# Performance work log

Hardware: AMD Instinct MI355X
Metric: run time of the kernel (lower is better)

Reference implementation:

```python
import jax, jax.numpy as jnp
import numpy as np

DIM = 256
HEADS = 4
DIM_HEAD = 32
HIDDEN = HEADS * DIM_HEAD  # 128
SCALE = DIM_HEAD ** -0.5
EPS = 1e-5


def setup_inputs() -> dict:
    key = jax.random.key(0)
    ks = jax.random.split(key, 6)
    b, h, w = 4, 64, 64
    x = jax.random.normal(ks[0], (b, DIM, h, w), dtype=jnp.float32)
    # GroupNorm(1, dim) affine params
    gamma = jnp.ones((DIM,), dtype=jnp.float32)
    beta = jnp.zeros((DIM,), dtype=jnp.float32)
    # 1x1 convs as dense matrices over channels
    w_qkv = jax.random.normal(ks[1], (3 * HIDDEN, DIM), dtype=jnp.float32) * (DIM ** -0.5)
    w_out = jax.random.normal(ks[2], (DIM, HIDDEN), dtype=jnp.float32) * (HIDDEN ** -0.5)
    b_out = jax.random.normal(ks[3], (DIM,), dtype=jnp.float32) * 0.02
    return {"x": x, "gamma": gamma, "beta": beta, "w_qkv": w_qkv,
            "w_out": w_out, "b_out": b_out}


def reference(x, gamma, beta, w_qkv, w_out, b_out):
    b, c, h, w = x.shape
    n = h * w
    # GroupNorm with 1 group == layernorm over (C,H,W) per sample, per-channel affine
    mu = jnp.mean(x, axis=(1, 2, 3), keepdims=True)
    var = jnp.var(x, axis=(1, 2, 3), keepdims=True)
    xn = (x - mu) * jax.lax.rsqrt(var + EPS)
    xn = xn * gamma[None, :, None, None] + beta[None, :, None, None]
    # 1x1 conv -> qkv, then split into heads; flatten spatial dims to n = h*w
    qkv = jnp.einsum('bchw,oc->bohw', xn, w_qkv)            # (b, 3*hidden, h, w)
    qkv = qkv.reshape(b, 3, HEADS, DIM_HEAD, n)
    q, k, v = qkv[:, 0], qkv[:, 1], qkv[:, 2]               # (b, heads, dim_head, n)
    q = q * SCALE
    sim = jnp.einsum('bhci,bhcj->bhij', q, k)               # (b, heads, n, n)
    attn = jax.nn.softmax(sim, axis=-1)                     # stable softmax (max subtract)
    out = jnp.einsum('bhij,bhcj->bhic', attn, v)            # (b, heads, n, dim_head)
    out = out.transpose(0, 1, 3, 2).reshape(b, HIDDEN, h, w)
    y = jnp.einsum('bchw,oc->bohw', out, w_out) + b_out[None, :, None, None]
    return y
```

## Files before the change

kernel.cpp:

```cpp
#include <hip/hip_runtime.h>
#include <math.h>

#define BATCH 4
#define CDIM 256
#define NPIX 4096
#define NPB (CDIM * NPIX)
#define HEADS 4
#define DH 32
#define HID 128
#define OQKV 384
#define QK_SCALE (0.1767766952966369f * 1.44269504088896340736f)
#define SOFTMAX_C 10.0f
#define LN_EPS 1e-5f

typedef _Float16 f16;
typedef _Float16 f16x8 __attribute__((ext_vector_type(8)));
typedef _Float16 f16x4 __attribute__((ext_vector_type(4)));
typedef float f32x4 __attribute__((ext_vector_type(4)));

__device__ __forceinline__ void gload16(const void* g, void* l) {
  __builtin_amdgcn_global_load_lds(
      (const __attribute__((address_space(1))) void*)g,
      (__attribute__((address_space(3))) void*)l, 16, 0, 0);
}

union U8u { unsigned int u[4]; f16x8 v; };
union U8h { f16 h[8]; f16x8 v; };

__global__ __launch_bounds__(256) void ln_reduce(const float* __restrict__ x,
                                                 float* __restrict__ part) {
  const int blk = blockIdx.x;
  const int b = blk >> 6;
  const int slice = blk & 63;
  const float4* xp = (const float4*)(x + (size_t)b * NPB) + (size_t)slice * 4096;
  const int t = threadIdx.x;
  float s = 0.f, ss = 0.f;
#pragma unroll
  for (int k = 0; k < 16; ++k) {
    float4 v = xp[t + k * 256];
    s += v.x + v.y + v.z + v.w;
    ss += v.x * v.x + v.y * v.y + v.z * v.z + v.w * v.w;
  }
#pragma unroll
  for (int d = 1; d < 64; d <<= 1) {
    s += __shfl_xor(s, d);
    ss += __shfl_xor(ss, d);
  }
  __shared__ float red[8];
  const int wv = t >> 6;
  if ((t & 63) == 0) { red[wv * 2] = s; red[wv * 2 + 1] = ss; }
  __syncthreads();
  if (t == 0) {
    part[blk * 2]     = red[0] + red[2] + red[4] + red[6];
    part[blk * 2 + 1] = red[1] + red[3] + red[5] + red[7];
  }
}

__global__ void ln_finalize(const float* __restrict__ part, float* __restrict__ stats) {
  const int t = threadIdx.x;
  const int b = t >> 6, lane = t & 63;
  float s  = part[(b * 64 + lane) * 2];
  float ss = part[(b * 64 + lane) * 2 + 1];
#pragma unroll
  for (int d = 1; d < 64; d <<= 1) {
    s += __shfl_xor(s, d);
    ss += __shfl_xor(ss, d);
  }
  if (lane == 0) {
    float mu = s * (1.f / (float)NPB);
    float var = ss * (1.f / (float)NPB) - mu * mu;
    stats[b * 2] = mu;
    stats[b * 2 + 1] = rsqrtf(var + LN_EPS);
  }
}

__global__ __launch_bounds__(256) void qkv_gemm(const float* __restrict__ x,
                                                const float* __restrict__ gamma,
                                                const float* __restrict__ beta,
                                                const float* __restrict__ wqkv,
                                                const float* __restrict__ stats,
                                                f16* __restrict__ qT,
                                                f16* __restrict__ kT,
                                                f16* __restrict__ vO) {
  const int b = blockIdx.z;
  const int oclass = blockIdx.y;
  const int p0 = blockIdx.x * 128;
  const int t = threadIdx.x;
  const int w = t >> 6, lane = t & 63, low4 = lane & 15, quad = lane >> 4;
  const int ow0 = (w >> 1) * 64, pw0 = (w & 1) * 64;
  const float mu = stats[2 * b], rstd = stats[2 * b + 1];
  const float wscale = (oclass == 0) ? QK_SCALE : 1.f;

  __shared__ f16 Ws[128 * 40];
  __shared__ float Xs[32 * 132];

  const int wo = t >> 1, wh = (t & 1) * 16;
  const int xc = t >> 3, xpq = (t & 7) * 16;
  const float* wg = wqkv + (size_t)(oclass * 128 + wo) * CDIM + wh;
  const float* xg = x + ((size_t)b * CDIM + xc) * NPIX + p0 + xpq;

  f32x4 acc[4][4] = {};
  f32x4 wr[4], xr[4];
  {
    const float ga = gamma[xc] * rstd;
    const float bb = beta[xc] - mu * ga;
#pragma unroll
    for (int j = 0; j < 4; ++j) {
      wr[j] = *(const f32x4*)(wg + j * 4);
      f32x4 r = *(const f32x4*)(xg + j * 4);
      r[0] = r[0] * ga + bb; r[1] = r[1] * ga + bb;
      r[2] = r[2] * ga + bb; r[3] = r[3] * ga + bb;
      xr[j] = r;
    }
  }

  for (int ks = 0; ks < 8; ++ks) {
    __syncthreads();
    {
      U8h h0, h1;
#pragma unroll
      for (int e = 0; e < 4; ++e) {
        h0.h[e]     = (f16)(wr[0][e] * wscale);
        h0.h[4 + e] = (f16)(wr[1][e] * wscale);
        h1.h[e]     = (f16)(wr[2][e] * wscale);
        h1.h[4 + e] = (f16)(wr[3][e] * wscale);
      }
      *(f16x8*)&Ws[wo * 40 + wh]     = h0.v;
      *(f16x8*)&Ws[wo * 40 + wh + 8] = h1.v;
#pragma unroll
      for (int j = 0; j < 4; ++j)
        *(f32x4*)&Xs[xc * 132 + xpq + 4 * j] = xr[j];
    }
    __syncthreads();

    if (ks < 7) {
      const int k0n = (ks + 1) * 32;
      const float ga = gamma[k0n + xc] * rstd;
      const float bb = beta[k0n + xc] - mu * ga;
#pragma unroll
      for (int j = 0; j < 4; ++j) {
        wr[j] = *(const f32x4*)(wg + k0n + j * 4);
        f32x4 r = *(const f32x4*)(xg + (size_t)k0n * NPIX + j * 4);
        r[0] = r[0] * ga + bb; r[1] = r[1] * ga + bb;
        r[2] = r[2] * ga + bb; r[3] = r[3] * ga + bb;
        xr[j] = r;
      }
    }

    f16x8 wf[4], xf[4];
#pragma unroll
    for (int i = 0; i < 4; ++i)
      wf[i] = *(const f16x8*)&Ws[(ow0 + i * 16 + low4) * 40 + quad * 8];
#pragma unroll
    for (int j = 0; j < 4; ++j) {
      const int pl = pw0 + j * 16 + low4;
      U8u xv;
#pragma unroll
      for (int r = 0; r < 4; ++r) {
        const float e0 = Xs[(quad * 8 + 2 * r) * 132 + pl];
        const float e1 = Xs[(quad * 8 + 2 * r + 1) * 132 + pl];
        xv.u[r] = __builtin_bit_cast(unsigned int,
                    __builtin_amdgcn_cvt_pkrtz(e0, e1));
      }
      xf[j] = xv.v;
    }

    if (oclass < 2) {
#pragma unroll
      for (int i = 0; i < 4; ++i)
#pragma unroll
        for (int j = 0; j < 4; ++j)
          acc[i][j] = __builtin_amdgcn_mfma_f32_16x16x32_f16(wf[i], xf[j], acc[i][j], 0, 0, 0);
    } else {
#pragma unroll
      for (int i = 0; i < 4; ++i)
#pragma unroll
        for (int j = 0; j < 4; ++j)
          acc[i][j] = __builtin_amdgcn_mfma_f32_16x16x32_f16(xf[i], wf[j], acc[i][j], 0, 0, 0);
    }
  }

  if (oclass < 2) {
    f16* dst = (oclass == 0) ? qT : kT;
#pragma unroll
    for (int i = 0; i < 4; ++i) {
      const int o_loc = ow0 + i * 16 + quad * 4;
      const int hh = o_loc >> 5;
      const int cb = o_loc & 31;
      f16* base = dst + ((size_t)(b * HEADS + hh) * NPIX) * DH + cb;
#pragma unroll
      for (int j = 0; j < 4; ++j) {
        const int p = p0 + pw0 + j * 16 + low4;
        f16x4 v = {(f16)acc[i][j][0], (f16)acc[i][j][1],
                   (f16)acc[i][j][2], (f16)acc[i][j][3]};
        *(f16x4*)(base + (size_t)p * DH) = v;
      }
    }
  } else {
#pragma unroll
    for (int j = 0; j < 4; ++j) {
      const int o_loc = ow0 + j * 16 + low4;
      const int hh = o_loc >> 5;
      const int cc = o_loc & 31;
      f16* base = vO + ((size_t)(b * HEADS + hh) * DH + cc) * NPIX;
#pragma unroll
      for (int i = 0; i < 4; ++i) {
        const int p = p0 + pw0 + i * 16 + quad * 4;
        f16x4 v = {(f16)acc[i][j][0], (f16)acc[i][j][1],
                   (f16)acc[i][j][2], (f16)acc[i][j][3]};
        *(f16x4*)(base + p) = v;
      }
    }
  }
}

__global__ __launch_bounds__(256, 4) void attn_kernel(const f16* __restrict__ qT,
                                                      const f16* __restrict__ kT,
                                                      const f16* __restrict__ vO,
                                                      f16* __restrict__ obufT) {
  const int bh_idx = blockIdx.x;
  const int i0 = blockIdx.y * 64;
  const int h = bh_idx & 3;
  const int b = bh_idx >> 2;
  const int t = threadIdx.x;
  const int w = t >> 6;
  const int lane = t & 63;
  const int low4 = lane & 15;
  const int quad = lane >> 4;

  __shared__ f16 Ks[2][2048];
  __shared__ f16 Vs[2][2048];

  const size_t bh = (size_t)(b * HEADS + h);
  const f16* kTb = kT + bh * NPIX * DH;
  const f16* vb  = vO + bh * DH * NPIX;

  const int vn = w * 64 + lane;
  const int vc = vn >> 3;
  const int vjc = (vn & 7) ^ (vc & 7);
  const f16* vgbase = vb + (size_t)vc * NPIX + vjc * 8;
  const int krow = w * 16 + (lane >> 2);
  const int kchk = (lane & 3) ^ ((lane >> 3) & 3);
  const f16* kgbase = kTb + (size_t)krow * DH + kchk * 8;

  const f16x8 qf = *(const f16x8*)(qT + (bh * NPIX + i0 + w * 16 + low4) * DH + quad * 8);

  f32x4 ov0 = {0, 0, 0, 0}, ov1 = {0, 0, 0, 0};
  float lp = 0.f;
  const f32x4 cinit = {-SOFTMAX_C, -SOFTMAX_C, -SOFTMAX_C, -SOFTMAX_C};

  union U4 { unsigned int u[2]; f16x4 v; };

  auto stage = [&](int buf, int jt) {
    gload16(kgbase + (size_t)jt * DH, &Ks[buf][w * 512]);
    gload16(vgbase + jt,              &Vs[buf][w * 512]);
  };

  const int kread_chunk = (quad ^ ((low4 >> 1) & 3)) << 3;

  stage(0, 0);
  for (int it = 0; it < NPIX / 64; ++it) {
    const int cur = it & 1;
    __syncthreads();
    if (it + 1 < NPIX / 64) stage(cur ^ 1, (it + 1) * 64);

    f16x8 kf[4];
#pragma unroll
    for (int tt = 0; tt < 4; ++tt)
      kf[tt] = *(const f16x8*)&Ks[cur][(tt * 16 + low4) * 32 + kread_chunk];
    f16x4 va[4][2];
#pragma unroll
    for (int tt = 0; tt < 4; ++tt) {
      const int jc16 = tt * 2 + (quad >> 1);
      const int sub = (quad & 1) * 4;
      const int c0 = low4, c1 = low4 + 16;
      va[tt][0] = *(const f16x4*)&Vs[cur][(c0 * 8 + (jc16 ^ (c0 & 7))) * 8 + sub];
      va[tt][1] = *(const f16x4*)&Vs[cur][(c1 * 8 + (jc16 ^ (c1 & 7))) * 8 + sub];
    }

    f32x4 st[4];
    __builtin_amdgcn_s_setprio(1);
#pragma unroll
    for (int tt = 0; tt < 4; ++tt)
      st[tt] = __builtin_amdgcn_mfma_f32_16x16x32_f16(kf[tt], qf, cinit, 0, 0, 0);
    __builtin_amdgcn_s_setprio(0);

    U4 pb[4];
#pragma unroll
    for (int tt = 0; tt < 4; ++tt) {
      const float a0 = __builtin_amdgcn_exp2f(st[tt][0]);
      const float a1 = __builtin_amdgcn_exp2f(st[tt][1]);
      const float a2 = __builtin_amdgcn_exp2f(st[tt][2]);
      const float a3 = __builtin_amdgcn_exp2f(st[tt][3]);
      lp += (a0 + a1) + (a2 + a3);
      pb[tt].u[0] = __builtin_bit_cast(unsigned int, __builtin_amdgcn_cvt_pkrtz(a0, a1));
      pb[tt].u[1] = __builtin_bit_cast(unsigned int, __builtin_amdgcn_cvt_pkrtz(a2, a3));
    }

    __builtin_amdgcn_s_setprio(1);
#pragma unroll
    for (int tt = 0; tt < 4; ++tt) {
      ov0 = __builtin_amdgcn_mfma_f32_16x16x16f16(va[tt][0], pb[tt].v, ov0, 0, 0, 0);
      ov1 = __builtin_amdgcn_mfma_f32_16x16x16f16(va[tt][1], pb[tt].v, ov1, 0, 0, 0);
    }
    __builtin_amdgcn_s_setprio(0);
  }

  lp += __shfl_xor(lp, 16);
  lp += __shfl_xor(lp, 32);
  const float inv = 1.f / lp;

  const int pix0 = i0 + w * 16 + low4;
  f16* ob = obufT + ((size_t)b * NPIX + pix0) * HID + h * DH + 4 * quad;
  {
    f16x4 v0 = {(f16)(ov0[0] * inv), (f16)(ov0[1] * inv), (f16)(ov0[2] * inv), (f16)(ov0[3] * inv)};
    f16x4 v1 = {(f16)(ov1[0] * inv), (f16)(ov1[1] * inv), (f16)(ov1[2] * inv), (f16)(ov1[3] * inv)};
    *(f16x4*)(ob)      = v0;
    *(f16x4*)(ob + 16) = v1;
  }
}

__global__ __launch_bounds__(256) void out_gemm(const f16* __restrict__ obufT,
                                                const float* __restrict__ wout,
                                                const float* __restrict__ bout,
                                                float* __restrict__ y) {
  const int b = blockIdx.z;
  const int o0 = blockIdx.y * 128;
  const int p0 = blockIdx.x * 128;
  const int t = threadIdx.x;
  const int w = t >> 6, lane = t & 63, low4 = lane & 15, quad = lane >> 4;
  const int ow0 = (w >> 1) * 64, pw0 = (w & 1) * 64;

  __shared__ f16 Ws2[128 * 136];

  {
    const int ro = t >> 1, half = (t & 1) * 64;
    const float* wg = wout + (size_t)(o0 + ro) * HID + half;
#pragma unroll
    for (int jj = 0; jj < 8; ++jj) {
      f32x4 a = *(const f32x4*)(wg + jj * 8);
      f32x4 c = *(const f32x4*)(wg + jj * 8 + 4);
      U8h hv;
      hv.h[0]=(f16)a[0]; hv.h[1]=(f16)a[1]; hv.h[2]=(f16)a[2]; hv.h[3]=(f16)a[3];
      hv.h[4]=(f16)c[0]; hv.h[5]=(f16)c[1]; hv.h[6]=(f16)c[2]; hv.h[7]=(f16)c[3];
      *(f16x8*)&Ws2[ro * 136 + half + jj * 8] = hv.v;
    }
  }
  __syncthreads();

  const f16* bg = obufT + ((size_t)b * NPIX + p0) * HID;

  f32x4 acc[4][4] = {};
#pragma unroll
  for (int ks = 0; ks < 4; ++ks) {
    const int k0 = ks * 32;
    f16x8 af[4], bf[4];
#pragma unroll
    for (int j = 0; j < 4; ++j)
      bf[j] = *(const f16x8*)(bg + (size_t)(pw0 + j * 16 + low4) * HID + k0 + quad * 8);
#pragma unroll
    for (int i = 0; i < 4; ++i)
      af[i] = *(const f16x8*)&Ws2[(ow0 + i * 16 + low4) * 136 + k0 + quad * 8];
#pragma unroll
    for (int i = 0; i < 4; ++i)
#pragma unroll
      for (int j = 0; j < 4; ++j)
        acc[i][j] = __builtin_amdgcn_mfma_f32_16x16x32_f16(af[i], bf[j], acc[i][j], 0, 0, 0);
  }

#pragma unroll
  for (int i = 0; i < 4; ++i) {
    const int ob = o0 + ow0 + i * 16 + quad * 4;
    const float b0v = bout[ob], b1v = bout[ob + 1], b2v = bout[ob + 2], b3v = bout[ob + 3];
    float* yb = y + ((size_t)b * CDIM + ob) * NPIX + p0 + pw0 + low4;
#pragma unroll
    for (int j = 0; j < 4; ++j) {
      yb[j * 16]                       = acc[i][j][0] + b0v;
      yb[(size_t)NPIX + j * 16]       = acc[i][j][1] + b1v;
      yb[(size_t)2 * NPIX + j * 16]   = acc[i][j][2] + b2v;
      yb[(size_t)3 * NPIX + j * 16]   = acc[i][j][3] + b3v;
    }
  }
}

extern "C" void kernel_launch(void* const* d_in, const int* in_sizes, int n_in,
                              void* d_out, int out_size, void* d_ws, size_t ws_size,
                              hipStream_t stream) {
  const float* x     = (const float*)d_in[0];
  const float* gamma = (const float*)d_in[1];
  const float* beta  = (const float*)d_in[2];
  const float* wqkv  = (const float*)d_in[3];
  const float* wout  = (const float*)d_in[4];
  const float* bout  = (const float*)d_in[5];
  float* y = (float*)d_out;

  char* wsb = (char*)d_ws;
  float* part  = (float*)wsb;
  float* stats = part + 512;
  f16* qT = (f16*)(wsb + 4096);
  f16* kT = qT + (size_t)BATCH * HEADS * NPIX * DH;
  f16* vO = kT + (size_t)BATCH * HEADS * NPIX * DH;
  f16* obufT = vO + (size_t)BATCH * HEADS * NPIX * DH;

  ln_reduce<<<dim3(256), 256, 0, stream>>>(x, part);
  ln_finalize<<<dim3(1), 256, 0, stream>>>(part, stats);
  qkv_gemm<<<dim3(32, 3, BATCH), 256, 0, stream>>>(x, gamma, beta, wqkv, stats, qT, kT, vO);
  attn_kernel<<<dim3(16, 64), 256, 0, stream>>>(qT, kT, vO, obufT);
  out_gemm<<<dim3(32, 2, BATCH), 256, 0, stream>>>(obufT, wout, bout, y);
}
```

Measured before the change: 159.8 us.

## Split attention keys across waves with register-direct loads and LDS combine

Each wave now takes a quarter of the key/value sequence for all 64 queries of the block, instead of every wave sweeping all keys for its own 16 queries. K and V fragments are loaded straight from global memory into double-buffered registers, which removes the LDS staging and the per-tile __syncthreads. Partial outputs and row sums from the four waves are reduced through shared memory at the end. The trade-offs are more registers (launch bounds lowered to 3) and less coalesced global loads that depend on the L2 cache rather than on LDS reuse.

```diff
diff --git a/kernel.cpp b/kernel.cpp
--- a/kernel.cpp
+++ b/kernel.cpp
@@ -214,7 +214,7 @@
   }
 }
 
-__global__ __launch_bounds__(256, 4) void attn_kernel(const f16* __restrict__ qT,
+__global__ __launch_bounds__(256, 3) void attn_kernel(const f16* __restrict__ qT,
                                                       const f16* __restrict__ kT,
                                                       const f16* __restrict__ vO,
                                                       f16* __restrict__ obufT) {
@@ -228,93 +228,107 @@
   const int low4 = lane & 15;
   const int quad = lane >> 4;
 
-  __shared__ f16 Ks[2][2048];
-  __shared__ f16 Vs[2][2048];
-
   const size_t bh = (size_t)(b * HEADS + h);
   const f16* kTb = kT + bh * NPIX * DH;
   const f16* vb  = vO + bh * DH * NPIX;
 
-  const int vn = w * 64 + lane;
-  const int vc = vn >> 3;
-  const int vjc = (vn & 7) ^ (vc & 7);
-  const f16* vgbase = vb + (size_t)vc * NPIX + vjc * 8;
-  const int krow = w * 16 + (lane >> 2);
-  const int kchk = (lane & 3) ^ ((lane >> 3) & 3);
-  const f16* kgbase = kTb + (size_t)krow * DH + kchk * 8;
-
-  const f16x8 qf = *(const f16x8*)(qT + (bh * NPIX + i0 + w * 16 + low4) * DH + quad * 8);
-
-  f32x4 ov0 = {0, 0, 0, 0}, ov1 = {0, 0, 0, 0};
-  float lp = 0.f;
+  f16x8 qf[4];
+#pragma unroll
+  for (int qg = 0; qg < 4; ++qg)
+    qf[qg] = *(const f16x8*)(qT + (bh * NPIX + i0 + qg * 16 + low4) * DH + quad * 8);
+
+  f32x4 ov[4][2] = {};
+  float lp[4] = {0.f, 0.f, 0.f, 0.f};
   const f32x4 cinit = {-SOFTMAX_C, -SOFTMAX_C, -SOFTMAX_C, -SOFTMAX_C};
 
   union U4 { unsigned int u[2]; f16x4 v; };
 
-  auto stage = [&](int buf, int jt) {
-    gload16(kgbase + (size_t)jt * DH, &Ks[buf][w * 512]);
-    gload16(vgbase + jt,              &Vs[buf][w * 512]);
-  };
-
-  const int kread_chunk = (quad ^ ((low4 >> 1) & 3)) << 3;
-
-  stage(0, 0);
-  for (int it = 0; it < NPIX / 64; ++it) {
-    const int cur = it & 1;
-    __syncthreads();
-    if (it + 1 < NPIX / 64) stage(cur ^ 1, (it + 1) * 64);
-
-    f16x8 kf[4];
-#pragma unroll
-    for (int tt = 0; tt < 4; ++tt)
-      kf[tt] = *(const f16x8*)&Ks[cur][(tt * 16 + low4) * 32 + kread_chunk];
-    f16x4 va[4][2];
-#pragma unroll
-    for (int tt = 0; tt < 4; ++tt) {
-      const int jc16 = tt * 2 + (quad >> 1);
-      const int sub = (quad & 1) * 4;
-      const int c0 = low4, c1 = low4 + 16;
-      va[tt][0] = *(const f16x4*)&Vs[cur][(c0 * 8 + (jc16 ^ (c0 & 7))) * 8 + sub];
-      va[tt][1] = *(const f16x4*)&Vs[cur][(c1 * 8 + (jc16 ^ (c1 & 7))) * 8 + sub];
-    }
-
-    f32x4 st[4];
-    __builtin_amdgcn_s_setprio(1);
-#pragma unroll
-    for (int tt = 0; tt < 4; ++tt)
-      st[tt] = __builtin_amdgcn_mfma_f32_16x16x32_f16(kf[tt], qf, cinit, 0, 0, 0);
-    __builtin_amdgcn_s_setprio(0);
-
-    U4 pb[4];
-#pragma unroll
-    for (int tt = 0; tt < 4; ++tt) {
-      const float a0 = __builtin_amdgcn_exp2f(st[tt][0]);
-      const float a1 = __builtin_amdgcn_exp2f(st[tt][1]);
-      const float a2 = __builtin_amdgcn_exp2f(st[tt][2]);
-      const float a3 = __builtin_amdgcn_exp2f(st[tt][3]);
-      lp += (a0 + a1) + (a2 + a3);
-      pb[tt].u[0] = __builtin_bit_cast(unsigned int, __builtin_amdgcn_cvt_pkrtz(a0, a1));
-      pb[tt].u[1] = __builtin_bit_cast(unsigned int, __builtin_amdgcn_cvt_pkrtz(a2, a3));
-    }
-
-    __builtin_amdgcn_s_setprio(1);
-#pragma unroll
-    for (int tt = 0; tt < 4; ++tt) {
-      ov0 = __builtin_amdgcn_mfma_f32_16x16x16f16(va[tt][0], pb[tt].v, ov0, 0, 0, 0);
-      ov1 = __builtin_amdgcn_mfma_f32_16x16x16f16(va[tt][1], pb[tt].v, ov1, 0, 0, 0);
-    }
-    __builtin_amdgcn_s_setprio(0);
-  }
-
-  lp += __shfl_xor(lp, 16);
-  lp += __shfl_xor(lp, 32);
-  const float inv = 1.f / lp;
-
-  const int pix0 = i0 + w * 16 + low4;
-  f16* ob = obufT + ((size_t)b * NPIX + pix0) * HID + h * DH + 4 * quad;
+  const int j0w = w * (NPIX / 4);
+  const f16* kg  = kTb + (size_t)(j0w + low4) * DH + quad * 8;
+  const f16* vg0 = vb + (size_t)low4 * NPIX + j0w + quad * 4;
+  const f16* vg1 = vb + (size_t)(16 + low4) * NPIX + j0w + quad * 4;
+
+  f16x8 kf[2][2];
+  f16x4 va[2][2][2];
+  kf[0][0] = *(const f16x8*)(kg);
+  kf[0][1] = *(const f16x8*)(kg + (size_t)16 * DH);
+  va[0][0][0] = *(const f16x4*)(vg0);
+  va[0][1][0] = *(const f16x4*)(vg0 + 16);
+  va[0][0][1] = *(const f16x4*)(vg1);
+  va[0][1][1] = *(const f16x4*)(vg1 + 16);
+
+#pragma unroll 2
+  for (int it = 0; it < 32; ++it) {
+    const int cb = it & 1;
+    if (it + 1 < 32) {
+      const int off = (it + 1) * 32;
+      kf[cb ^ 1][0] = *(const f16x8*)(kg + (size_t)off * DH);
+      kf[cb ^ 1][1] = *(const f16x8*)(kg + (size_t)(off + 16) * DH);
+      va[cb ^ 1][0][0] = *(const f16x4*)(vg0 + off);
+      va[cb ^ 1][1][0] = *(const f16x4*)(vg0 + off + 16);
+      va[cb ^ 1][0][1] = *(const f16x4*)(vg1 + off);
+      va[cb ^ 1][1][1] = *(const f16x4*)(vg1 + off + 16);
+    }
+
+#pragma unroll
+    for (int qg = 0; qg < 4; ++qg) {
+      f32x4 st0 = __builtin_amdgcn_mfma_f32_16x16x32_f16(kf[cb][0], qf[qg], cinit, 0, 0, 0);
+      f32x4 st1 = __builtin_amdgcn_mfma_f32_16x16x32_f16(kf[cb][1], qf[qg], cinit, 0, 0, 0);
+
+      U4 pb0, pb1;
+      const float a0 = __builtin_amdgcn_exp2f(st0[0]);
+      const float a1 = __builtin_amdgcn_exp2f(st0[1]);
+      const float a2 = __builtin_amdgcn_exp2f(st0[2]);
+      const float a3 = __builtin_amdgcn_exp2f(st0[3]);
+      lp[qg] += (a0 + a1) + (a2 + a3);
+      pb0.u[0] = __builtin_bit_cast(unsigned int, __builtin_amdgcn_cvt_pkrtz(a0, a1));
+      pb0.u[1] = __builtin_bit_cast(unsigned int, __builtin_amdgcn_cvt_pkrtz(a2, a3));
+      const float b0 = __builtin_amdgcn_exp2f(st1[0]);
+      const float b1 = __builtin_amdgcn_exp2f(st1[1]);
+      const float b2 = __builtin_amdgcn_exp2f(st1[2]);
+      const float b3 = __builtin_amdgcn_exp2f(st1[3]);
+      lp[qg] += (b0 + b1) + (b2 + b3);
+      pb1.u[0] = __builtin_bit_cast(unsigned int, __builtin_amdgcn_cvt_pkrtz(b0, b1));
+      pb1.u[1] = __builtin_bit_cast(unsigned int, __builtin_amdgcn_cvt_pkrtz(b2, b3));
+
+      ov[qg][0] = __builtin_amdgcn_mfma_f32_16x16x16f16(va[cb][0][0], pb0.v, ov[qg][0], 0, 0, 0);
+      ov[qg][0] = __builtin_amdgcn_mfma_f32_16x16x16f16(va[cb][1][0], pb1.v, ov[qg][0], 0, 0, 0);
+      ov[qg][1] = __builtin_amdgcn_mfma_f32_16x16x16f16(va[cb][0][1], pb0.v, ov[qg][1], 0, 0, 0);
+      ov[qg][1] = __builtin_amdgcn_mfma_f32_16x16x16f16(va[cb][1][1], pb1.v, ov[qg][1], 0, 0, 0);
+    }
+  }
+
+#pragma unroll
+  for (int qg = 0; qg < 4; ++qg) {
+    lp[qg] += __shfl_xor(lp[qg], 16);
+    lp[qg] += __shfl_xor(lp[qg], 32);
+  }
+
+  __shared__ float Cmb[4][2048];
+  __shared__ float Lps[4][4][16];
+#pragma unroll
+  for (int qg = 0; qg < 4; ++qg) {
+#pragma unroll
+    for (int ch = 0; ch < 2; ++ch)
+      *(f32x4*)&Cmb[w][((qg * 2 + ch) * 64 + lane) * 4] = ov[qg][ch];
+    if (quad == 0) Lps[w][qg][low4] = lp[qg];
+  }
+  __syncthreads();
+
+  const float lpt = ((Lps[0][w][low4] + Lps[1][w][low4]) +
+                     (Lps[2][w][low4] + Lps[3][w][low4]));
+  const float inv = 1.f / lpt;
+  f32x4 o0 = {0, 0, 0, 0}, o1 = {0, 0, 0, 0};
+#pragma unroll
+  for (int u = 0; u < 4; ++u) {
+    o0 += *(const f32x4*)&Cmb[u][((w * 2 + 0) * 64 + lane) * 4];
+    o1 += *(const f32x4*)&Cmb[u][((w * 2 + 1) * 64 + lane) * 4];
+  }
+
+  f16* ob = obufT + ((size_t)b * NPIX + i0 + w * 16 + low4) * HID + h * DH + 4 * quad;
   {
-    f16x4 v0 = {(f16)(ov0[0] * inv), (f16)(ov0[1] * inv), (f16)(ov0[2] * inv), (f16)(ov0[3] * inv)};
-    f16x4 v1 = {(f16)(ov1[0] * inv), (f16)(ov1[1] * inv), (f16)(ov1[2] * inv), (f16)(ov1[3] * inv)};
+    f16x4 v0 = {(f16)(o0[0] * inv), (f16)(o0[1] * inv), (f16)(o0[2] * inv), (f16)(o0[3] * inv)};
+    f16x4 v1 = {(f16)(o1[0] * inv), (f16)(o1[1] * inv), (f16)(o1[2] * inv), (f16)(o1[3] * inv)};
     *(f16x4*)(ob)      = v0;
     *(f16x4*)(ob + 16) = v1;
   }
```

New measurement: 196.6 us. +23.0%, slower.

## Split key tiles across waves and reduce partial attention outputs in LDS

Applied to the files above, without the earlier changes.

Each wave now owns a 16-key slice of every 64-key tile for all 64 queries, instead of owning 16 queries over all keys. This cuts per-wave LDS reads of K and V by a factor of four. The cost is holding four Q fragments and eight output accumulators per wave, plus a cross-wave reduction of partial outputs and row sums through LDS at the end. Register pressure rises, which may hurt occupancy under the 4-blocks launch bound.

```diff
diff --git a/kernel.cpp b/kernel.cpp
--- a/kernel.cpp
+++ b/kernel.cpp
@@ -228,8 +228,11 @@
   const int low4 = lane & 15;
   const int quad = lane >> 4;
 
-  __shared__ f16 Ks[2][2048];
-  __shared__ f16 Vs[2][2048];
+  union SharedU {
+    struct { f16 Ks[2][2048]; f16 Vs[2][2048]; } s;
+    struct { float Cmb[4][8][256]; float Lps[4][4][16]; } c;
+  };
+  __shared__ SharedU sh;
 
   const size_t bh = (size_t)(b * HEADS + h);
   const f16* kTb = kT + bh * NPIX * DH;
@@ -243,20 +246,27 @@
   const int kchk = (lane & 3) ^ ((lane >> 3) & 3);
   const f16* kgbase = kTb + (size_t)krow * DH + kchk * 8;
 
-  const f16x8 qf = *(const f16x8*)(qT + (bh * NPIX + i0 + w * 16 + low4) * DH + quad * 8);
-
-  f32x4 ov0 = {0, 0, 0, 0}, ov1 = {0, 0, 0, 0};
-  float lp = 0.f;
+  f16x8 qf[4];
+#pragma unroll
+  for (int qg = 0; qg < 4; ++qg)
+    qf[qg] = *(const f16x8*)(qT + (bh * NPIX + i0 + qg * 16 + low4) * DH + quad * 8);
+
+  f32x4 ov[4][2] = {};
+  float lp[4] = {0.f, 0.f, 0.f, 0.f};
   const f32x4 cinit = {-SOFTMAX_C, -SOFTMAX_C, -SOFTMAX_C, -SOFTMAX_C};
 
   union U4 { unsigned int u[2]; f16x4 v; };
 
   auto stage = [&](int buf, int jt) {
-    gload16(kgbase + (size_t)jt * DH, &Ks[buf][w * 512]);
-    gload16(vgbase + jt,              &Vs[buf][w * 512]);
+    gload16(kgbase + (size_t)jt * DH, &sh.s.Ks[buf][w * 512]);
+    gload16(vgbase + jt,              &sh.s.Vs[buf][w * 512]);
   };
 
-  const int kread_chunk = (quad ^ ((low4 >> 1) & 3)) << 3;
+  const int kread_off = (w * 16 + low4) * 32 + ((quad ^ ((low4 >> 1) & 3)) << 3);
+  const int jc16 = w * 2 + (quad >> 1);
+  const int sub = (quad & 1) * 4;
+  const int va_off0 = (low4 * 8 + (jc16 ^ (low4 & 7))) * 8 + sub;
+  const int va_off1 = ((16 + low4) * 8 + (jc16 ^ ((16 + low4) & 7))) * 8 + sub;
 
   stage(0, 0);
   for (int it = 0; it < NPIX / 64; ++it) {
@@ -264,57 +274,68 @@
     __syncthreads();
     if (it + 1 < NPIX / 64) stage(cur ^ 1, (it + 1) * 64);
 
-    f16x8 kf[4];
-#pragma unroll
-    for (int tt = 0; tt < 4; ++tt)
-      kf[tt] = *(const f16x8*)&Ks[cur][(tt * 16 + low4) * 32 + kread_chunk];
-    f16x4 va[4][2];
-#pragma unroll
-    for (int tt = 0; tt < 4; ++tt) {
-      const int jc16 = tt * 2 + (quad >> 1);
-      const int sub = (quad & 1) * 4;
-      const int c0 = low4, c1 = low4 + 16;
-      va[tt][0] = *(const f16x4*)&Vs[cur][(c0 * 8 + (jc16 ^ (c0 & 7))) * 8 + sub];
-      va[tt][1] = *(const f16x4*)&Vs[cur][(c1 * 8 + (jc16 ^ (c1 & 7))) * 8 + sub];
-    }
+    const f16x8 kf  = *(const f16x8*)&sh.s.Ks[cur][kread_off];
+    const f16x4 va0 = *(const f16x4*)&sh.s.Vs[cur][va_off0];
+    const f16x4 va1 = *(const f16x4*)&sh.s.Vs[cur][va_off1];
 
     f32x4 st[4];
     __builtin_amdgcn_s_setprio(1);
 #pragma unroll
-    for (int tt = 0; tt < 4; ++tt)
-      st[tt] = __builtin_amdgcn_mfma_f32_16x16x32_f16(kf[tt], qf, cinit, 0, 0, 0);
+    for (int qg = 0; qg < 4; ++qg)
+      st[qg] = __builtin_amdgcn_mfma_f32_16x16x32_f16(kf, qf[qg], cinit, 0, 0, 0);
     __builtin_amdgcn_s_setprio(0);
 
     U4 pb[4];
 #pragma unroll
-    for (int tt = 0; tt < 4; ++tt) {
-      const float a0 = __builtin_amdgcn_exp2f(st[tt][0]);
-      const float a1 = __builtin_amdgcn_exp2f(st[tt][1]);
-      const float a2 = __builtin_amdgcn_exp2f(st[tt][2]);
-      const float a3 = __builtin_amdgcn_exp2f(st[tt][3]);
-      lp += (a0 + a1) + (a2 + a3);
-      pb[tt].u[0] = __builtin_bit_cast(unsigned int, __builtin_amdgcn_cvt_pkrtz(a0, a1));
-      pb[tt].u[1] = __builtin_bit_cast(unsigned int, __builtin_amdgcn_cvt_pkrtz(a2, a3));
+    for (int qg = 0; qg < 4; ++qg) {
+      const float a0 = __builtin_amdgcn_exp2f(st[qg][0]);
+      const float a1 = __builtin_amdgcn_exp2f(st[qg][1]);
+      const float a2 = __builtin_amdgcn_exp2f(st[qg][2]);
+      const float a3 = __builtin_amdgcn_exp2f(st[qg][3]);
+      lp[qg] += (a0 + a1) + (a2 + a3);
+      pb[qg].u[0] = __builtin_bit_cast(unsigned int, __builtin_amdgcn_cvt_pkrtz(a0, a1));
+      pb[qg].u[1] = __builtin_bit_cast(unsigned int, __builtin_amdgcn_cvt_pkrtz(a2, a3));
     }
 
     __builtin_amdgcn_s_setprio(1);
 #pragma unroll
-    for (int tt = 0; tt < 4; ++tt) {
-      ov0 = __builtin_amdgcn_mfma_f32_16x16x16f16(va[tt][0], pb[tt].v, ov0, 0, 0, 0);
-      ov1 = __builtin_amdgcn_mfma_f32_16x16x16f16(va[tt][1], pb[tt].v, ov1, 0, 0, 0);
+    for (int qg = 0; qg < 4; ++qg) {
+      ov[qg][0] = __builtin_amdgcn_mfma_f32_16x16x16f16(va0, pb[qg].v, ov[qg][0], 0, 0, 0);
+      ov[qg][1] = __builtin_amdgcn_mfma_f32_16x16x16f16(va1, pb[qg].v, ov[qg][1], 0, 0, 0);
     }
     __builtin_amdgcn_s_setprio(0);
   }
 
-  lp += __shfl_xor(lp, 16);
-  lp += __shfl_xor(lp, 32);
-  const float inv = 1.f / lp;
-
-  const int pix0 = i0 + w * 16 + low4;
-  f16* ob = obufT + ((size_t)b * NPIX + pix0) * HID + h * DH + 4 * quad;
+#pragma unroll
+  for (int qg = 0; qg < 4; ++qg) {
+    lp[qg] += __shfl_xor(lp[qg], 16);
+    lp[qg] += __shfl_xor(lp[qg], 32);
+  }
+
+  __syncthreads();
+#pragma unroll
+  for (int qg = 0; qg < 4; ++qg) {
+#pragma unroll
+    for (int ch = 0; ch < 2; ++ch)
+      *(f32x4*)&sh.c.Cmb[w][qg * 2 + ch][lane * 4] = ov[qg][ch];
+    if (quad == 0) sh.c.Lps[w][qg][low4] = lp[qg];
+  }
+  __syncthreads();
+
+  const float lpt = ((sh.c.Lps[0][w][low4] + sh.c.Lps[1][w][low4]) +
+                     (sh.c.Lps[2][w][low4] + sh.c.Lps[3][w][low4]));
+  const float inv = 1.f / lpt;
+  f32x4 o0 = {0, 0, 0, 0}, o1 = {0, 0, 0, 0};
+#pragma unroll
+  for (int u = 0; u < 4; ++u) {
+    o0 += *(const f32x4*)&sh.c.Cmb[u][w * 2 + 0][lane * 4];
+    o1 += *(const f32x4*)&sh.c.Cmb[u][w * 2 + 1][lane * 4];
+  }
+
+  f16* ob = obufT + ((size_t)b * NPIX + i0 + w * 16 + low4) * HID + h * DH + 4 * quad;
   {
-    f16x4 v0 = {(f16)(ov0[0] * inv), (f16)(ov0[1] * inv), (f16)(ov0[2] * inv), (f16)(ov0[3] * inv)};
-    f16x4 v1 = {(f16)(ov1[0] * inv), (f16)(ov1[1] * inv), (f16)(ov1[2] * inv), (f16)(ov1[3] * inv)};
+    f16x4 v0 = {(f16)(o0[0] * inv), (f16)(o0[1] * inv), (f16)(o0[2] * inv), (f16)(o0[3] * inv)};
+    f16x4 v1 = {(f16)(o1[0] * inv), (f16)(o1[1] * inv), (f16)(o1[2] * inv), (f16)(o1[3] * inv)};
     *(f16x4*)(ob)      = v0;
     *(f16x4*)(ob + 16) = v1;
   }
```

New measurement: 164.0 us. +2.6%, slower.
